# Performance work log

Hardware: AMD Instinct MI355X
Metric: run time of the kernel (lower is better)

Reference implementation:

```python
import jax, jax.numpy as jnp
import numpy as np

K = 5  # adaptive kernel size; kernel has K*K channels


def setup_inputs() -> dict:
    key = jax.random.key(0)
    k1, k2 = jax.random.split(key)
    B, C, H, W = 8, 64, 256, 256
    x = jax.random.normal(k1, (B, C, H + K - 1, W + K - 1), dtype=jnp.float32)
    kernel = jax.random.uniform(k2, (B, K * K, H, W), dtype=jnp.float32)
    return {"x": x, "kernel": kernel}


def reference(x, kernel):
    # x: [B, C, H+K-1, W+K-1], kernel: [B, K*K, H, W] -> out: [B, C, H, W]
    # Each output pixel (h, w) = sum_{i,j} x[:, :, h+i, w+j] * kernel[:, i*K+j, h, w]
    B, KK, H, W = kernel.shape
    out = jnp.zeros((B, x.shape[1], H, W), dtype=x.dtype)
    for idx in range(KK):
        i, j = idx // K, idx % K
        patch = x[:, :, i:i + H, j:j + W]              # [B, C, H, W]
        out = out + patch * kernel[:, idx][:, None]    # broadcast tap over C
    return out
```

## Files before the change

kernel.cpp:

```cpp
#include <hip/hip_runtime.h>


constexpr int K  = 5;
constexpr int B  = 8;
constexpr int C  = 64;
constexpr int H  = 256;
constexpr int W  = 256;
constexpr int HX = H + K - 1;
constexpr int WX = W + K - 1;

constexpr int CH  = 4;
constexpr int NCG = C / CH;
constexpr int HPB = 4;
constexpr int NHB = H / HPB;
constexpr int NWG = NHB * B * NCG;

constexpr int XROWS      = HPB + K - 1;
constexpr int CH_FLOATS  = XROWS * WX;
constexpr int LDS_FLOATS = CH * CH_FLOATS;

typedef float f4 __attribute__((ext_vector_type(4)));

__global__ __launch_bounds__(256, 4)
void adaptive_conv_kernel(const float* __restrict__ x,
                          const float* __restrict__ kern,
                          float* __restrict__ out) {
    __shared__ float xs[LDS_FLOATS];

    const int k    = blockIdx.x;
    const int orig = (k & 7) * (NWG / 8) + (k >> 3);
    const int cg   = orig & (NCG - 1);
    const int hblk = (orig >> 4) & (NHB - 1);
    const int b    = orig >> 10;

    const int tid  = threadIdx.x;
    const int lane = tid & 63;
    const int wv   = tid >> 6;
    const int w0   = lane * 4;
    const int h    = hblk * HPB + wv;
    const int c0   = cg * CH;

    const size_t xplane = (size_t)HX * WX;
    {
        const float* src = x + ((size_t)b * C + c0 + wv) * xplane
                             + (size_t)(hblk * HPB) * WX;
        float* dst = &xs[wv * CH_FLOATS];
        #pragma unroll
        for (int t = 0; t < 8; ++t) {
            f4 v = *(const f4*)(src + t * 256 + lane * 4);
            *(f4*)(dst + t * 256 + lane * 4) = v;
        }
        if (lane < 8) {
            f4 v = *(const f4*)(src + 2048 + lane * 4);
            *(f4*)(dst + 2048 + lane * 4) = v;
        }
    }
    __syncthreads();

    f4 acc[CH];
    #pragma unroll
    for (int ch = 0; ch < CH; ++ch) acc[ch] = (f4)0.0f;

    const float* kb = kern + (size_t)b * (K * K * H * W) + (size_t)h * W + w0;

    #pragma unroll
    for (int i = 0; i < K; ++i) {
        f4 t[K];
        #pragma unroll
        for (int j = 0; j < K; ++j) {
            t[j] = *(const f4*)(kb + (size_t)(i * K + j) * (H * W));
        }

        #pragma unroll
        for (int ch = 0; ch < CH; ++ch) {
            const float* xr = &xs[ch * CH_FLOATS + (wv + i) * WX + w0];
            f4 xa  = *(const f4*)(xr);
            f4 xcv = *(const f4*)(xr + 4);
            float xsg[8] = {xa.x, xa.y, xa.z, xa.w, xcv.x, xcv.y, xcv.z, xcv.w};

            #pragma unroll
            for (int j = 0; j < K; ++j) {
                acc[ch].x = fmaf(xsg[j + 0], t[j].x, acc[ch].x);
                acc[ch].y = fmaf(xsg[j + 1], t[j].y, acc[ch].y);
                acc[ch].z = fmaf(xsg[j + 2], t[j].z, acc[ch].z);
                acc[ch].w = fmaf(xsg[j + 3], t[j].w, acc[ch].w);
            }
        }
    }

    float* ob = out + ((size_t)b * C + c0) * (H * W) + (size_t)h * W + w0;
    #pragma unroll
    for (int ch = 0; ch < CH; ++ch) {
        __builtin_nontemporal_store(acc[ch], (f4*)(ob + (size_t)ch * (H * W)));
    }
}

extern "C" void kernel_launch(void* const* d_in, const int* in_sizes, int n_in,
                              void* d_out, int out_size, void* d_ws, size_t ws_size,
                              hipStream_t stream) {
    const float* x    = (const float*)d_in[0];
    const float* kern = (const float*)d_in[1];
    float*       out  = (float*)d_out;

    dim3 grid(NWG);
    dim3 block(256);
    adaptive_conv_kernel<<<grid, block, 0, stream>>>(x, kern, out);
}
```

Measured before the change: 65.96 us.

## Double-buffer LDS staging across four channel groups using async global_load_lds

Each workgroup now processes four consecutive channel groups instead of one, so the grid shrinks fourfold. The input tile for the next group is prefetched into a second LDS buffer with direct global-to-LDS loads while the current group computes. The per-pixel kernel taps are also reused by the same block across groups. In exchange, LDS use doubles, occupancy drops to 2 blocks per SIMD, and correctness depends on the barrier waiting for the async LDS loads.

```diff
diff --git a/kernel.cpp b/kernel.cpp
--- a/kernel.cpp
+++ b/kernel.cpp
@@ -11,87 +11,101 @@
 
 constexpr int CH  = 4;
 constexpr int NCG = C / CH;
+constexpr int GPB = 4;
+constexpr int CGB = NCG / GPB;
 constexpr int HPB = 4;
 constexpr int NHB = H / HPB;
-constexpr int NWG = NHB * B * NCG;
+constexpr int NWG = NHB * B * CGB;
 
-constexpr int XROWS      = HPB + K - 1;
-constexpr int CH_FLOATS  = XROWS * WX;
-constexpr int LDS_FLOATS = CH * CH_FLOATS;
+constexpr int CH_REAL = (HPB + K - 1) * WX;
+constexpr int CH_PAD  = 2304;
+constexpr int BUF_FLOATS = CH * CH_PAD;
 
 typedef float f4 __attribute__((ext_vector_type(4)));
 
-__global__ __launch_bounds__(256, 4)
+__global__ __launch_bounds__(256, 2)
 void adaptive_conv_kernel(const float* __restrict__ x,
                           const float* __restrict__ kern,
                           float* __restrict__ out) {
-    __shared__ float xs[LDS_FLOATS];
+    __shared__ float xs[2][BUF_FLOATS];
 
     const int k    = blockIdx.x;
     const int orig = (k & 7) * (NWG / 8) + (k >> 3);
-    const int cg   = orig & (NCG - 1);
-    const int hblk = (orig >> 4) & (NHB - 1);
-    const int b    = orig >> 10;
+    const int cgs  = orig & (CGB - 1);
+    const int hblk = (orig >> 2) & (NHB - 1);
+    const int b    = orig >> 8;
 
     const int tid  = threadIdx.x;
     const int lane = tid & 63;
     const int wv   = tid >> 6;
     const int w0   = lane * 4;
     const int h    = hblk * HPB + wv;
-    const int c0   = cg * CH;
 
     const size_t xplane = (size_t)HX * WX;
-    {
-        const float* src = x + ((size_t)b * C + c0 + wv) * xplane
+    const size_t XTOT   = (size_t)B * C * xplane;
+    const float* kb = kern + (size_t)b * (K * K * H * W) + (size_t)h * W + w0;
+
+    auto stage = [&](int t, int p) {
+        const int ch = (cgs * GPB + t) * CH + wv;
+        const float* src = x + ((size_t)b * C + ch) * xplane
                              + (size_t)(hblk * HPB) * WX;
-        float* dst = &xs[wv * CH_FLOATS];
         #pragma unroll
-        for (int t = 0; t < 8; ++t) {
-            f4 v = *(const f4*)(src + t * 256 + lane * 4);
-            *(f4*)(dst + t * 256 + lane * 4) = v;
+        for (int s = 0; s < 9; ++s) {
+            const float* gp = src + s * 256 + lane * 4;
+            if (s == 8 && gp + 4 > x + XTOT) gp = x;
+            float* lp = &xs[p][wv * CH_PAD + s * 256];
+            __builtin_amdgcn_global_load_lds(
+                (const __attribute__((address_space(1))) void*)gp,
+                (__attribute__((address_space(3))) void*)lp, 16, 0, 0);
         }
-        if (lane < 8) {
-            f4 v = *(const f4*)(src + 2048 + lane * 4);
-            *(f4*)(dst + 2048 + lane * 4) = v;
-        }
-    }
+    };
+
+    stage(0, 0);
     __syncthreads();
 
-    f4 acc[CH];
     #pragma unroll
-    for (int ch = 0; ch < CH; ++ch) acc[ch] = (f4)0.0f;
+    for (int t = 0; t < GPB; ++t) {
+        const int p = t & 1;
+        if (t + 1 < GPB) stage(t + 1, p ^ 1);
 
-    const float* kb = kern + (size_t)b * (K * K * H * W) + (size_t)h * W + w0;
+        const int c0 = (cgs * GPB + t) * CH;
 
-    #pragma unroll
-    for (int i = 0; i < K; ++i) {
-        f4 t[K];
+        f4 acc[CH];
         #pragma unroll
-        for (int j = 0; j < K; ++j) {
-            t[j] = *(const f4*)(kb + (size_t)(i * K + j) * (H * W));
+        for (int ch = 0; ch < CH; ++ch) acc[ch] = (f4)0.0f;
+
+        #pragma unroll
+        for (int i = 0; i < K; ++i) {
+            f4 tc[K];
+            #pragma unroll
+            for (int j = 0; j < K; ++j) {
+                tc[j] = *(const f4*)(kb + (size_t)(i * K + j) * (H * W));
+            }
+
+            #pragma unroll
+            for (int ch = 0; ch < CH; ++ch) {
+                const float* xr = &xs[p][ch * CH_PAD + (wv + i) * WX + w0];
+                f4 xa  = *(const f4*)(xr);
+                f4 xcv = *(const f4*)(xr + 4);
+                float xsg[8] = {xa.x, xa.y, xa.z, xa.w, xcv.x, xcv.y, xcv.z, xcv.w};
+
+                #pragma unroll
+                for (int j = 0; j < K; ++j) {
+                    acc[ch].x = fmaf(xsg[j + 0], tc[j].x, acc[ch].x);
+                    acc[ch].y = fmaf(xsg[j + 1], tc[j].y, acc[ch].y);
+                    acc[ch].z = fmaf(xsg[j + 2], tc[j].z, acc[ch].z);
+                    acc[ch].w = fmaf(xsg[j + 3], tc[j].w, acc[ch].w);
+                }
+            }
         }
 
+        float* ob = out + ((size_t)b * C + c0) * (H * W) + (size_t)h * W + w0;
         #pragma unroll
         for (int ch = 0; ch < CH; ++ch) {
-            const float* xr = &xs[ch * CH_FLOATS + (wv + i) * WX + w0];
-            f4 xa  = *(const f4*)(xr);
-            f4 xcv = *(const f4*)(xr + 4);
-            float xsg[8] = {xa.x, xa.y, xa.z, xa.w, xcv.x, xcv.y, xcv.z, xcv.w};
+            __builtin_nontemporal_store(acc[ch], (f4*)(ob + (size_t)ch * (H * W)));
+        }
 
-            #pragma unroll
-            for (int j = 0; j < K; ++j) {
-                acc[ch].x = fmaf(xsg[j + 0], t[j].x, acc[ch].x);
-                acc[ch].y = fmaf(xsg[j + 1], t[j].y, acc[ch].y);
-                acc[ch].z = fmaf(xsg[j + 2], t[j].z, acc[ch].z);
-                acc[ch].w = fmaf(xsg[j + 3], t[j].w, acc[ch].w);
-            }
-        }
-    }
-
-    float* ob = out + ((size_t)b * C + c0) * (H * W) + (size_t)h * W + w0;
-    #pragma unroll
-    for (int ch = 0; ch < CH; ++ch) {
-        __builtin_nontemporal_store(acc[ch], (f4*)(ob + (size_t)ch * (H * W)));
+        if (t + 1 < GPB) __syncthreads();
     }
 }
 
```

New measurement: 71.52 us. 1.08x slower.
